# Optimization experiments

Measured on AMD Instinct MI355X. Metric: run time of the kernel, lower is better.

## Reference

```python
import jax, jax.numpy as jnp
import numpy as np

HIDDEN = 2048
N_HEADS = 16
HEAD_DIM = HIDDEN // N_HEADS
ROPE_THETA = 10000.0
BSZ, SEQ = 2, 2048
NEG_INF = -1e9


def setup_inputs() -> dict:
    key = jax.random.key(0)
    ks = jax.random.split(key, 5)
    scale = 1.0 / np.sqrt(HIDDEN)
    hidden_states = jax.random.normal(ks[0], (BSZ, SEQ, HIDDEN), dtype=jnp.float32)
    Wq = jax.random.normal(ks[1], (HIDDEN, HIDDEN), dtype=jnp.float32) * scale
    Wk = jax.random.normal(ks[2], (HIDDEN, HIDDEN), dtype=jnp.float32) * scale
    Wv = jax.random.normal(ks[3], (HIDDEN, HIDDEN), dtype=jnp.float32) * scale
    Wo = jax.random.normal(ks[4], (HIDDEN, HIDDEN), dtype=jnp.float32) * scale
    # additive causal mask, [1, 1, S, S]
    causal = jnp.triu(jnp.full((SEQ, SEQ), NEG_INF, dtype=jnp.float32), k=1)
    attention_mask = causal[None, None, :, :]
    position_ids = jnp.arange(SEQ, dtype=jnp.int32)
    return {
        "hidden_states": hidden_states,
        "Wq": Wq, "Wk": Wk, "Wv": Wv, "Wo": Wo,
        "attention_mask": attention_mask,
        "position_ids": position_ids,
    }


def _rotate_half(x):
    half = x.shape[-1] // 2
    return jnp.concatenate((-x[..., half:], x[..., :half]), axis=-1)


def _rope_tables(seq_len, position_ids):
    # inv_freq: [head_dim/2]
    inv_freq = 1.0 / (ROPE_THETA ** (jnp.arange(0, HEAD_DIM, 2, dtype=jnp.float32) / HEAD_DIM))
    t = jnp.arange(seq_len, dtype=jnp.float32)
    freqs = t[:, None] * inv_freq[None, :]              # [S, D/2]
    emb = jnp.concatenate((freqs, freqs), axis=-1)      # [S, D]
    cos = jnp.cos(emb)[position_ids]                    # [S, D]
    sin = jnp.sin(emb)[position_ids]
    return cos, sin


def reference(hidden_states, Wq, Wk, Wv, Wo, attention_mask, position_ids):
    b, s, h = hidden_states.shape
    def proj(W):
        return (hidden_states @ W.T).reshape(b, s, N_HEADS, HEAD_DIM).transpose(0, 2, 1, 3)
    q = proj(Wq)  # [B, H, S, D]
    k = proj(Wk)
    v = proj(Wv)
    cos, sin = _rope_tables(s, position_ids)            # [S, D], broadcasts over B,H
    q = q * cos + _rotate_half(q) * sin
    k = k * cos + _rotate_half(k) * sin
    scores = jnp.einsum('bhqd,bhkd->bhqk', q, k) / np.sqrt(HEAD_DIM)
    scores = scores + attention_mask
    w = jax.nn.softmax(scores, axis=-1)
    out = jnp.einsum('bhqk,bhkd->bhqd', w, v)           # [B, H, S, D]
    out = out.transpose(0, 2, 1, 3).reshape(b, s, h)
    return out @ Wo.T
```

## Files before the change

### kernel.cpp

```cpp
#include <hip/hip_runtime.h>
#include <cstdint>
#include <cstddef>

typedef __bf16 bf16;
typedef __bf16 bf16x4 __attribute__((ext_vector_type(4)));
typedef __bf16 bf16x8 __attribute__((ext_vector_type(8)));
typedef float  f32x4  __attribute__((ext_vector_type(4)));
typedef short  s16x4  __attribute__((ext_vector_type(4)));

#define HIDDEN 2048
#define NHEADS 16
#define HDIM   128
#define BSZ    2
#define SEQ    2048
#define BS     (BSZ*SEQ)
#define QKW    (2*HIDDEN)

union b4u { bf16x4 h; s16x4 s; };

__device__ __forceinline__ void async16(const bf16* g, bf16* l) {
    __builtin_amdgcn_global_load_lds(
        (const __attribute__((address_space(1))) unsigned int*)g,
        (__attribute__((address_space(3))) unsigned int*)l, 16, 0, 0);
}

#define BARX()  asm volatile("s_barrier" ::: "memory")
#define VMW(N)  asm volatile("s_waitcnt vmcnt(" #N ")" ::: "memory")

__global__ __launch_bounds__(256) void cast_all(const float* __restrict__ hs,
                                                const float* __restrict__ Wq,
                                                const float* __restrict__ Wk,
                                                const float* __restrict__ Wv,
                                                const float* __restrict__ Wo,
                                                const int* __restrict__ pos,
                                                bf16* __restrict__ hs_b,
                                                bf16* __restrict__ wqkv,
                                                bf16* __restrict__ wo_b,
                                                float2* __restrict__ tab) {
    int i = blockIdx.x * 256 + threadIdx.x;
    if (i >= 6291456) {
        int j = i - 6291456;
        int s = j >> 6, p = j & 63;
        float t = (float)pos[s];
        float inv = expf(-(float)(2 * p) * (9.2103403719761836f / 128.0f));
        float sn, cs;
        sincosf(t * inv, &sn, &cs);
        tab[j] = make_float2(cs, sn);
        return;
    }
    const float* src; bf16* dst; int off;
    if (i < 2097152) { src = hs; dst = hs_b; off = i; }
    else {
        int j = i - 2097152;
        int r = j >> 20;
        off = j & 1048575;
        if      (r == 0) { src = Wq; dst = wqkv; }
        else if (r == 1) { src = Wk; dst = wqkv + (size_t)4194304; }
        else if (r == 2) { src = Wv; dst = wqkv + (size_t)8388608; }
        else             { src = Wo; dst = wo_b; }
    }
    const float4 v = ((const float4*)src)[off];
    bf16x4 o;
    o.x = (bf16)v.x; o.y = (bf16)v.y; o.z = (bf16)v.z; o.w = (bf16)v.w;
    ((bf16x4*)dst)[off] = o;
}

__device__ __forceinline__ int qk_perm(int n) {
    int wl = n >> 6, j = n & 63;
    return ((wl >> 1) << 7) | ((j >> 5) << 6) | ((wl & 1) << 5) | (j & 31);
}

#define QKV_TILE(T, DOSTAGE, VMN) do {                                          \
    const int bufR_ = (T) & 3;                                                  \
    const bf16* lAr = smem + bufR_ * 16384 + (wm * 128 + l15) * 32 + colE;      \
    const bf16* lBr = smem + bufR_ * 16384 + 8192 + (wn * 64 + l15) * 32 + colE;\
    bf16x8 bfr[4], af[4];                                                       \
    _Pragma("unroll") for (int nf = 0; nf < 4; ++nf)                            \
        bfr[nf] = *(const bf16x8*)(lBr + nf * 512);                             \
    _Pragma("unroll") for (int mf = 0; mf < 4; ++mf)                            \
        af[mf] = *(const bf16x8*)(lAr + mf * 512);                              \
    if (DOSTAGE) {                                                              \
        bf16* dA = smem + (((T) + 3) & 3) * 16384 + w * 512;                    \
        async16(pa0 + ((T) + 3) * 32, dA);                                      \
        async16(pa1 + ((T) + 3) * 32, dA + 4096);                               \
    }                                                                           \
    BARX();                                                                     \
    __builtin_amdgcn_s_setprio(1);                                              \
    _Pragma("unroll") for (int mf = 0; mf < 4; ++mf)                            \
    _Pragma("unroll") for (int nf = 0; nf < 4; ++nf)                            \
        acc[mf][nf] = __builtin_amdgcn_mfma_f32_16x16x32_bf16(                  \
            af[mf], bfr[nf], acc[mf][nf], 0, 0, 0);                             \
    __builtin_amdgcn_s_setprio(0);                                              \
    BARX();                                                                     \
    _Pragma("unroll") for (int mf = 0; mf < 4; ++mf)                            \
        af[mf] = *(const bf16x8*)(lAr + 2048 + mf * 512);                       \
    if (DOSTAGE) {                                                              \
        bf16* dB = smem + (((T) + 3) & 3) * 16384 + 8192 + w * 512;             \
        async16(pb0 + ((T) + 3) * 32, dB);                                      \
        async16(pb1 + ((T) + 3) * 32, dB + 4096);                               \
    }                                                                           \
    VMW(VMN);                                                                   \
    BARX();                                                                     \
    __builtin_amdgcn_s_setprio(1);                                              \
    _Pragma("unroll") for (int mf = 0; mf < 4; ++mf)                            \
    _Pragma("unroll") for (int nf = 0; nf < 4; ++nf)                            \
        acc[4 + mf][nf] = __builtin_amdgcn_mfma_f32_16x16x32_bf16(              \
            af[mf], bfr[nf], acc[4 + mf][nf], 0, 0, 0);                         \
    __builtin_amdgcn_s_setprio(0);                                              \
    BARX();                                                                     \
} while (0)

__global__ __launch_bounds__(512, 2) void gemm_qkv(const bf16* __restrict__ A,
                                                   const bf16* __restrict__ Bt,
                                                   const float2* __restrict__ tab,
                                                   bf16* __restrict__ qk,
                                                   bf16* __restrict__ vtb) {
    __shared__ alignas(16) bf16 smem[65536];

    const int tid  = threadIdx.x;
    const int lane = tid & 63;
    const int w    = tid >> 6;
    const int l15  = lane & 15;
    const int quad = lane >> 4;
    const int wm   = w >> 2;
    const int wn   = w & 3;

    int raw = blockIdx.y * 24 + blockIdx.x;
    int wg  = (raw & 7) * 48 + (raw >> 3);
    const int mTile = (wg / 24) * 256;
    const int nTile = (wg % 24) * 256;

    const int sRow  = w * 16 + (lane >> 2);
    const int sColE = ((lane & 3) * 8) ^ ((lane & 32) ? 16 : 0);
    const bf16* pa0 = A + (size_t)(mTile + sRow) * HIDDEN + sColE;
    const bf16* pa1 = pa0 + (size_t)128 * HIDDEN;
    int n0 = sRow, n1 = sRow + 128;
    if (nTile < QKW) { n0 = qk_perm(n0); n1 = qk_perm(n1); }
    const bf16* pb0 = Bt + (size_t)(nTile + n0) * HIDDEN + sColE;
    const bf16* pb1 = Bt + (size_t)(nTile + n1) * HIDDEN + sColE;

    const int colE = (quad * 8) ^ ((l15 & 8) ? 16 : 0);

    f32x4 acc[8][4];
#pragma unroll
    for (int i = 0; i < 8; ++i)
#pragma unroll
        for (int j = 0; j < 4; ++j) acc[i][j] = (f32x4){0.f, 0.f, 0.f, 0.f};

#pragma unroll
    for (int tt = 0; tt < 3; ++tt) {
        bf16* dA = smem + tt * 16384 + w * 512;
        async16(pa0 + tt * 32, dA);
        async16(pa1 + tt * 32, dA + 4096);
        async16(pb0 + tt * 32, dA + 8192);
        async16(pb1 + tt * 32, dA + 8192 + 4096);
    }
    VMW(8);
    BARX();

#pragma unroll 4
    for (int t = 0; t < 60; ++t) QKV_TILE(t, 1, 8);
    QKV_TILE(60, 1, 8);
    QKV_TILE(61, 0, 4);
    QKV_TILE(62, 0, 0);
    QKV_TILE(63, 0, 0);

    if (nTile < QKW) {
        const int hbase = nTile + (wn >> 1) * 128 + (wn & 1) * 32;
#pragma unroll
        for (int mf = 0; mf < 8; ++mf)
#pragma unroll
            for (int r = 0; r < 4; ++r) {
                int row = mTile + wm * 128 + mf * 16 + quad * 4 + r;
                int s   = row & (SEQ - 1);
                float2 t0 = tab[s * 64 + (wn & 1) * 32 + l15];
                float2 t1 = tab[s * 64 + (wn & 1) * 32 + 16 + l15];
                size_t rb = (size_t)row * QKW + hbase + l15;
                float lo0 = acc[mf][0][r], hi0 = acc[mf][2][r];
                float lo1 = acc[mf][1][r], hi1 = acc[mf][3][r];
                qk[rb]      = (bf16)(lo0 * t0.x - hi0 * t0.y);
                qk[rb + 64] = (bf16)(hi0 * t0.x + lo0 * t0.y);
                qk[rb + 16] = (bf16)(lo1 * t1.x - hi1 * t1.y);
                qk[rb + 80] = (bf16)(hi1 * t1.x + lo1 * t1.y);
            }
    } else {
#pragma unroll
        for (int mf = 0; mf < 8; ++mf)
#pragma unroll
            for (int nf = 0; nf < 4; ++nf) {
                int col_v = (nTile - QKW) + wn * 64 + nf * 16 + l15;
                int row0  = mTile + wm * 128 + mf * 16 + quad * 4;
                bf16x4 pk;
#pragma unroll
                for (int r = 0; r < 4; ++r) pk[r] = (bf16)acc[mf][nf][r];
                *(bf16x4*)(vtb + (size_t)col_v * BS + row0) = pk;
            }
    }
}

template <typename OutT>
__global__ __launch_bounds__(256) void gemm_bt(const bf16* __restrict__ A,
                                               const bf16* __restrict__ Bt,
                                               OutT* __restrict__ C,
                                               int M, int N, int K) {
    __shared__ bf16 Als[128 * 32];
    __shared__ bf16 Bls[128 * 32];
    const int tid  = threadIdx.x;
    const int lane = tid & 63;
    const int w    = tid >> 6;
    const int l15  = lane & 15;
    const int quad = lane >> 4;
    const int mTile = blockIdx.y * 128;
    const int nTile = blockIdx.x * 128;
    const int wm = (w >> 1) * 64;
    const int wn = (w & 1) * 64;

    f32x4 acc[4][4];
#pragma unroll
    for (int i = 0; i < 4; ++i)
#pragma unroll
        for (int j = 0; j < 4; ++j) acc[i][j] = (f32x4){0.f, 0.f, 0.f, 0.f};

    const bf16* gA = A + (size_t)(mTile + w * 32 + (lane >> 2)) * K + (lane & 3) * 8;
    const bf16* gB = Bt + (size_t)(nTile + w * 32 + (lane >> 2)) * K + (lane & 3) * 8;
    bf16* lA = Als + w * 1024;
    bf16* lB = Bls + w * 1024;

    for (int k0 = 0; k0 < K; k0 += 32) {
        async16(gA + k0,          lA);
        async16(gA + 16 * K + k0, lA + 512);
        async16(gB + k0,          lB);
        async16(gB + 16 * K + k0, lB + 512);
        __syncthreads();

        bf16x8 af[4], bfr[4];
#pragma unroll
        for (int mi = 0; mi < 4; ++mi)
            af[mi] = *(const bf16x8*)(Als + (wm + mi * 16 + l15) * 32 + quad * 8);
#pragma unroll
        for (int ni = 0; ni < 4; ++ni)
            bfr[ni] = *(const bf16x8*)(Bls + (wn + ni * 16 + l15) * 32 + quad * 8);
#pragma unroll
        for (int mi = 0; mi < 4; ++mi)
#pragma unroll
            for (int ni = 0; ni < 4; ++ni)
                acc[mi][ni] = __builtin_amdgcn_mfma_f32_16x16x32_bf16(
                    af[mi], bfr[ni], acc[mi][ni], 0, 0, 0);
        __syncthreads();
    }

#pragma unroll
    for (int mi = 0; mi < 4; ++mi)
#pragma unroll
        for (int ni = 0; ni < 4; ++ni)
#pragma unroll
            for (int r = 0; r < 4; ++r) {
                int row = mTile + wm + mi * 16 + quad * 4 + r;
                int col = nTile + wn + ni * 16 + l15;
                C[(size_t)row * N + col] = (OutT)acc[mi][ni][r];
            }
}

__global__ __launch_bounds__(256) void attn_kernel(const bf16* __restrict__ qk,
                                                   const bf16* __restrict__ vt,
                                                   bf16* __restrict__ ao) {
    __shared__ bf16 Kls[64 * 128];
    __shared__ bf16 Vls[128 * 64];

    const int tid  = threadIdx.x;
    const int lane = tid & 63;
    const int w    = tid >> 6;
    const int l15  = lane & 15;
    const int quad = lane >> 4;
    const int bid  = blockIdx.x;
    const int qt   = 31 - (bid >> 5);
    const int bh   = bid & 31;
    const int b    = bh >> 4;
    const int h    = bh & 15;
    const int qbase = qt * 64;
    const size_t seq0 = (size_t)b * SEQ;

    bf16x8 qf[4];
    {
        const bf16* qp = qk + (seq0 + qbase + w * 16 + l15) * QKW + h * HDIM + quad * 8;
#pragma unroll
        for (int ks = 0; ks < 4; ++ks) qf[ks] = *(const bf16x8*)(qp + ks * 32);
    }

    f32x4 o[8];
#pragma unroll
    for (int i = 0; i < 8; ++i) o[i] = (f32x4){0.f, 0.f, 0.f, 0.f};
    float m_s = -3e38f, l_s = 0.f;
    const int qg = qbase + w * 16 + l15;

    const int krow = lane >> 4;
    const int kp   = lane & 15;
    const int vrow = lane >> 3;
    const int vp   = lane & 7;
    const int sw   = l15 & 7;

    for (int t = 0; t <= qt; ++t) {
        const int kb = t * 64;
#pragma unroll
        for (int i = 0; i < 4; ++i) {
            int j = w * 16 + i * 4 + krow;
            int c = (kp & 8) | ((kp & 7) ^ (j & 7));
            async16(qk + (seq0 + kb + j) * QKW + HIDDEN + h * HDIM + c * 8,
                    Kls + (w * 4 + i) * 512);
        }
#pragma unroll
        for (int i = 0; i < 4; ++i) {
            int d = w * 32 + i * 8 + vrow;
            int c = vp ^ (d & 7);
            async16(vt + (size_t)(h * HDIM + d) * (size_t)BS + seq0 + kb + c * 8,
                    Vls + (w * 4 + i) * 512);
        }
        __syncthreads();

        f32x4 sa[4];
#pragma unroll
        for (int ni = 0; ni < 4; ++ni) sa[ni] = (f32x4){0.f, 0.f, 0.f, 0.f};
#pragma unroll
        for (int ni = 0; ni < 4; ++ni)
#pragma unroll
            for (int ks = 0; ks < 4; ++ks) {
                bf16x8 kf = *(const bf16x8*)(Kls + (ni * 16 + l15) * 128 +
                                             (((ks * 4 + quad) ^ sw) << 3));
                sa[ni] = __builtin_amdgcn_mfma_f32_16x16x32_bf16(kf, qf[ks], sa[ni], 0, 0, 0);
            }

        const float scale = 0.08838834764831845f * 1.4426950408889634f;
        float rmax = -3e38f;
        const bool diag = (t == qt);
#pragma unroll
        for (int ni = 0; ni < 4; ++ni)
#pragma unroll
            for (int r = 0; r < 4; ++r) {
                float sv = sa[ni][r] * scale;
                if (diag) {
                    int jg = kb + ni * 16 + quad * 4 + r;
                    if (jg > qg) sv = -1e30f;
                }
                sa[ni][r] = sv;
                rmax = fmaxf(rmax, sv);
            }
        rmax = fmaxf(rmax, __shfl_xor(rmax, 16));
        rmax = fmaxf(rmax, __shfl_xor(rmax, 32));

        float mn = fmaxf(m_s, rmax);
        float alpha = exp2f(m_s - mn);
        m_s = mn;
        float rsum = 0.f;
        b4u pb[4];
#pragma unroll
        for (int ni = 0; ni < 4; ++ni)
#pragma unroll
            for (int r = 0; r < 4; ++r) {
                float e = exp2f(sa[ni][r] - mn);
                rsum += e;
                pb[ni].h[r] = (bf16)e;
            }
        rsum += __shfl_xor(rsum, 16);
        rsum += __shfl_xor(rsum, 32);
        l_s = l_s * alpha + rsum;

        if (__ballot(alpha != 1.f) != 0ull) {
#pragma unroll
            for (int n2 = 0; n2 < 8; ++n2)
#pragma unroll
                for (int r = 0; r < 4; ++r) o[n2][r] *= alpha;
        }

#pragma unroll
        for (int n2 = 0; n2 < 8; ++n2)
#pragma unroll
            for (int ni = 0; ni < 4; ++ni) {
                b4u vf;
                vf.h = *(const bf16x4*)(Vls + (n2 * 16 + l15) * 64 +
                                        ((((ni * 2 + (quad >> 1)) ^ sw) << 3) + (quad & 1) * 4));
                o[n2] = __builtin_amdgcn_mfma_f32_16x16x16bf16_1k(vf.s, pb[ni].s, o[n2], 0, 0, 0);
            }
        __syncthreads();
    }

    const float inv = 1.0f / l_s;
    bf16* op = ao + (seq0 + qg) * HIDDEN + h * HDIM + quad * 4;
#pragma unroll
    for (int n2 = 0; n2 < 8; ++n2) {
        bf16x4 pk;
#pragma unroll
        for (int r = 0; r < 4; ++r) pk[r] = (bf16)(o[n2][r] * inv);
        *(bf16x4*)(op + n2 * 16) = pk;
    }
}

extern "C" void kernel_launch(void* const* d_in, const int* in_sizes, int n_in,
                              void* d_out, int out_size, void* d_ws, size_t ws_size,
                              hipStream_t stream) {
    const float* hs = (const float*)d_in[0];
    const float* Wq = (const float*)d_in[1];
    const float* Wk = (const float*)d_in[2];
    const float* Wv = (const float*)d_in[3];
    const float* Wo = (const float*)d_in[4];
    const int* pos  = (const int*)d_in[6];
    float* out = (float*)d_out;

    bf16* hs_b = (bf16*)d_ws;
    bf16* wqkv = hs_b + (size_t)8388608;
    bf16* wo_b = wqkv + (size_t)12582912;
    bf16* qkb  = wo_b + (size_t)4194304;
    bf16* vtb  = qkb + (size_t)16777216;
    bf16* ao   = vtb + (size_t)8388608;
    float2* tab = (float2*)ao;

    cast_all<<<25088, 256, 0, stream>>>(hs, Wq, Wk, Wv, Wo, pos, hs_b, wqkv, wo_b, tab);
    gemm_qkv<<<dim3(24, 16), 512, 0, stream>>>(hs_b, wqkv, tab, qkb, vtb);
    attn_kernel<<<1024, 256, 0, stream>>>(qkb, vtb, ao);
    gemm_bt<float><<<dim3(HIDDEN / 128, BS / 128), 256, 0, stream>>>(ao, wo_b, out, BS, HIDDEN, HIDDEN);
}
```

Measured before the change: 408.4 us.

## Pipeline output GEMM with 4-stage async LDS and trim QKV barriers

Replaces the simple single-buffered output projection GEMM with a 128x256-tile, 512-thread kernel using a 4-deep global_load_lds ring buffer. The kernel waits on loads and synchronises once per k-step, matching the QKV GEMM. The QKV GEMM tile loop also drops from four barriers per k-step to one, placed at the start. Its block-to-tile mapping is remapped to a 1D grid so blocks sharing a weight slice are grouped per XCD for L2 reuse. This aims to hide load latency and cut barrier overhead, at the cost of more LDS per block and tighter reliance on ring-buffer distance for correctness.

```diff
diff --git a/kernel.cpp b/kernel.cpp
--- a/kernel.cpp
+++ b/kernel.cpp
@@ -71,9 +71,10 @@
 }
 
 #define QKV_TILE(T, DOSTAGE, VMN) do {                                          \
-    const int bufR_ = (T) & 3;                                                  \
-    const bf16* lAr = smem + bufR_ * 16384 + (wm * 128 + l15) * 32 + colE;      \
-    const bf16* lBr = smem + bufR_ * 16384 + 8192 + (wn * 64 + l15) * 32 + colE;\
+    VMW(VMN);                                                                   \
+    BARX();                                                                     \
+    const bf16* lAr = lA0 + ((T) & 3) * 16384;                                  \
+    const bf16* lBr = lB0 + ((T) & 3) * 16384;                                  \
     bf16x8 bfr[4], af[4];                                                       \
     _Pragma("unroll") for (int nf = 0; nf < 4; ++nf)                            \
         bfr[nf] = *(const bf16x8*)(lBr + nf * 512);                             \
@@ -84,14 +85,12 @@
         async16(pa0 + ((T) + 3) * 32, dA);                                      \
         async16(pa1 + ((T) + 3) * 32, dA + 4096);                               \
     }                                                                           \
-    BARX();                                                                     \
     __builtin_amdgcn_s_setprio(1);                                              \
     _Pragma("unroll") for (int mf = 0; mf < 4; ++mf)                            \
     _Pragma("unroll") for (int nf = 0; nf < 4; ++nf)                            \
         acc[mf][nf] = __builtin_amdgcn_mfma_f32_16x16x32_bf16(                  \
             af[mf], bfr[nf], acc[mf][nf], 0, 0, 0);                             \
     __builtin_amdgcn_s_setprio(0);                                              \
-    BARX();                                                                     \
     _Pragma("unroll") for (int mf = 0; mf < 4; ++mf)                            \
         af[mf] = *(const bf16x8*)(lAr + 2048 + mf * 512);                       \
     if (DOSTAGE) {                                                              \
@@ -99,15 +98,12 @@
         async16(pb0 + ((T) + 3) * 32, dB);                                      \
         async16(pb1 + ((T) + 3) * 32, dB + 4096);                               \
     }                                                                           \
-    VMW(VMN);                                                                   \
-    BARX();                                                                     \
     __builtin_amdgcn_s_setprio(1);                                              \
     _Pragma("unroll") for (int mf = 0; mf < 4; ++mf)                            \
     _Pragma("unroll") for (int nf = 0; nf < 4; ++nf)                            \
         acc[4 + mf][nf] = __builtin_amdgcn_mfma_f32_16x16x32_bf16(              \
             af[mf], bfr[nf], acc[4 + mf][nf], 0, 0, 0);                         \
     __builtin_amdgcn_s_setprio(0);                                              \
-    BARX();                                                                     \
 } while (0)
 
 __global__ __launch_bounds__(512, 2) void gemm_qkv(const bf16* __restrict__ A,
@@ -125,10 +121,11 @@
     const int wm   = w >> 2;
     const int wn   = w & 3;
 
-    int raw = blockIdx.y * 24 + blockIdx.x;
-    int wg  = (raw & 7) * 48 + (raw >> 3);
-    const int mTile = (wg / 24) * 256;
-    const int nTile = (wg % 24) * 256;
+    const int raw = blockIdx.x;
+    const int xq  = raw & 7;
+    const int kq  = raw >> 3;
+    const int mTile = (kq & 15) * 256;
+    const int nTile = (3 * xq + (kq >> 4)) * 256;
 
     const int sRow  = w * 16 + (lane >> 2);
     const int sColE = ((lane & 3) * 8) ^ ((lane & 32) ? 16 : 0);
@@ -140,6 +137,8 @@
     const bf16* pb1 = Bt + (size_t)(nTile + n1) * HIDDEN + sColE;
 
     const int colE = (quad * 8) ^ ((l15 & 8) ? 16 : 0);
+    const bf16* lA0 = smem + (wm * 128 + l15) * 32 + colE;
+    const bf16* lB0 = smem + 8192 + (wn * 64 + l15) * 32 + colE;
 
     f32x4 acc[8][4];
 #pragma unroll
@@ -153,16 +152,14 @@
         async16(pa0 + tt * 32, dA);
         async16(pa1 + tt * 32, dA + 4096);
         async16(pb0 + tt * 32, dA + 8192);
-        async16(pb1 + tt * 32, dA + 8192 + 4096);
-    }
-    VMW(8);
-    BARX();
+        async16(pb1 + tt * 32, dA + 12288);
+    }
 
 #pragma unroll 4
     for (int t = 0; t < 60; ++t) QKV_TILE(t, 1, 8);
     QKV_TILE(60, 1, 8);
-    QKV_TILE(61, 0, 4);
-    QKV_TILE(62, 0, 0);
+    QKV_TILE(61, 0, 8);
+    QKV_TILE(62, 0, 4);
     QKV_TILE(63, 0, 0);
 
     if (nTile < QKW) {
@@ -198,22 +195,56 @@
     }
 }
 
-template <typename OutT>
-__global__ __launch_bounds__(256) void gemm_bt(const bf16* __restrict__ A,
-                                               const bf16* __restrict__ Bt,
-                                               OutT* __restrict__ C,
-                                               int M, int N, int K) {
-    __shared__ bf16 Als[128 * 32];
-    __shared__ bf16 Bls[128 * 32];
+#define OUT_TILE(T, DOSTAGE, VMN) do {                                          \
+    VMW(VMN);                                                                   \
+    BARX();                                                                     \
+    const bf16* lAr = lA0 + ((T) & 3) * 12288;                                  \
+    const bf16* lBr = lB0 + ((T) & 3) * 12288;                                  \
+    bf16x8 bfr[4], af[4];                                                       \
+    _Pragma("unroll") for (int nf = 0; nf < 4; ++nf)                            \
+        bfr[nf] = *(const bf16x8*)(lBr + nf * 512);                             \
+    _Pragma("unroll") for (int mf = 0; mf < 4; ++mf)                            \
+        af[mf] = *(const bf16x8*)(lAr + mf * 512);                              \
+    if (DOSTAGE) {                                                              \
+        bf16* dS = smem + (((T) + 3) & 3) * 12288 + w * 512;                    \
+        async16(pa0 + ((T) + 3) * 32, dS);                                      \
+        async16(pb0 + ((T) + 3) * 32, dS + 4096);                               \
+        async16(pb1 + ((T) + 3) * 32, dS + 8192);                               \
+    }                                                                           \
+    __builtin_amdgcn_s_setprio(1);                                              \
+    _Pragma("unroll") for (int mf = 0; mf < 4; ++mf)                            \
+    _Pragma("unroll") for (int nf = 0; nf < 4; ++nf)                            \
+        acc[mf][nf] = __builtin_amdgcn_mfma_f32_16x16x32_bf16(                  \
+            af[mf], bfr[nf], acc[mf][nf], 0, 0, 0);                             \
+    __builtin_amdgcn_s_setprio(0);                                              \
+} while (0)
+
+__global__ __launch_bounds__(512, 2) void gemm_out(const bf16* __restrict__ A,
+                                                   const bf16* __restrict__ Bt,
+                                                   float* __restrict__ C) {
+    __shared__ alignas(16) bf16 smem[49152];
+
     const int tid  = threadIdx.x;
     const int lane = tid & 63;
     const int w    = tid >> 6;
     const int l15  = lane & 15;
     const int quad = lane >> 4;
-    const int mTile = blockIdx.y * 128;
-    const int nTile = blockIdx.x * 128;
-    const int wm = (w >> 1) * 64;
-    const int wn = (w & 1) * 64;
+    const int wm   = w >> 2;
+    const int wn   = w & 3;
+
+    const int raw = blockIdx.x;
+    const int mTile = (raw >> 3) * 128;
+    const int nTile = (raw & 7) * 256;
+
+    const int sRow  = w * 16 + (lane >> 2);
+    const int sColE = ((lane & 3) * 8) ^ ((lane & 32) ? 16 : 0);
+    const bf16* pa0 = A + (size_t)(mTile + sRow) * HIDDEN + sColE;
+    const bf16* pb0 = Bt + (size_t)(nTile + sRow) * HIDDEN + sColE;
+    const bf16* pb1 = pb0 + (size_t)128 * HIDDEN;
+
+    const int colE = (quad * 8) ^ ((l15 & 8) ? 16 : 0);
+    const bf16* lA0 = smem + (wm * 64 + l15) * 32 + colE;
+    const bf16* lB0 = smem + 4096 + (wn * 64 + l15) * 32 + colE;
 
     f32x4 acc[4][4];
 #pragma unroll
@@ -221,43 +252,30 @@
 #pragma unroll
         for (int j = 0; j < 4; ++j) acc[i][j] = (f32x4){0.f, 0.f, 0.f, 0.f};
 
-    const bf16* gA = A + (size_t)(mTile + w * 32 + (lane >> 2)) * K + (lane & 3) * 8;
-    const bf16* gB = Bt + (size_t)(nTile + w * 32 + (lane >> 2)) * K + (lane & 3) * 8;
-    bf16* lA = Als + w * 1024;
-    bf16* lB = Bls + w * 1024;
-
-    for (int k0 = 0; k0 < K; k0 += 32) {
-        async16(gA + k0,          lA);
-        async16(gA + 16 * K + k0, lA + 512);
-        async16(gB + k0,          lB);
-        async16(gB + 16 * K + k0, lB + 512);
-        __syncthreads();
-
-        bf16x8 af[4], bfr[4];
-#pragma unroll
-        for (int mi = 0; mi < 4; ++mi)
-            af[mi] = *(const bf16x8*)(Als + (wm + mi * 16 + l15) * 32 + quad * 8);
-#pragma unroll
-        for (int ni = 0; ni < 4; ++ni)
-            bfr[ni] = *(const bf16x8*)(Bls + (wn + ni * 16 + l15) * 32 + quad * 8);
-#pragma unroll
-        for (int mi = 0; mi < 4; ++mi)
-#pragma unroll
-            for (int ni = 0; ni < 4; ++ni)
-                acc[mi][ni] = __builtin_amdgcn_mfma_f32_16x16x32_bf16(
-                    af[mi], bfr[ni], acc[mi][ni], 0, 0, 0);
-        __syncthreads();
-    }
-
-#pragma unroll
-    for (int mi = 0; mi < 4; ++mi)
-#pragma unroll
-        for (int ni = 0; ni < 4; ++ni)
+#pragma unroll
+    for (int tt = 0; tt < 3; ++tt) {
+        bf16* dS = smem + tt * 12288 + w * 512;
+        async16(pa0 + tt * 32, dS);
+        async16(pb0 + tt * 32, dS + 4096);
+        async16(pb1 + tt * 32, dS + 8192);
+    }
+
+#pragma unroll 4
+    for (int t = 0; t < 60; ++t) OUT_TILE(t, 1, 6);
+    OUT_TILE(60, 1, 6);
+    OUT_TILE(61, 0, 6);
+    OUT_TILE(62, 0, 3);
+    OUT_TILE(63, 0, 0);
+
+#pragma unroll
+    for (int mf = 0; mf < 4; ++mf)
+#pragma unroll
+        for (int nf = 0; nf < 4; ++nf)
 #pragma unroll
             for (int r = 0; r < 4; ++r) {
-                int row = mTile + wm + mi * 16 + quad * 4 + r;
-                int col = nTile + wn + ni * 16 + l15;
-                C[(size_t)row * N + col] = (OutT)acc[mi][ni][r];
+                int row = mTile + wm * 64 + mf * 16 + quad * 4 + r;
+                int col = nTile + wn * 64 + nf * 16 + l15;
+                C[(size_t)row * HIDDEN + col] = acc[mf][nf][r];
             }
 }
 
@@ -414,7 +432,7 @@
     float2* tab = (float2*)ao;
 
     cast_all<<<25088, 256, 0, stream>>>(hs, Wq, Wk, Wv, Wo, pos, hs_b, wqkv, wo_b, tab);
-    gemm_qkv<<<dim3(24, 16), 512, 0, stream>>>(hs_b, wqkv, tab, qkb, vtb);
+    gemm_qkv<<<384, 512, 0, stream>>>(hs_b, wqkv, tab, qkb, vtb);
     attn_kernel<<<1024, 256, 0, stream>>>(qkb, vtb, ao);
-    gemm_bt<float><<<dim3(HIDDEN / 128, BS / 128), 256, 0, stream>>>(ao, wo_b, out, BS, HIDDEN, HIDDEN);
-}
+    gemm_out<<<256, 512, 0, stream>>>(ao, wo_b, out);
+}
```

After: 371.7 us. -9.0%, faster.
